# Kernel optimization log

Measured on AMD Instinct MI355X. Metric: run time of the kernel, lower is better.

The kernel has to match this reference:

```python
import jax, jax.numpy as jnp
import numpy as np
from jax import lax

D_MODEL = 768
BATCH = 16
SEQ = 2048
N_BLOCKS = D_MODEL // 3
LN_EPS = 1e-5


def setup_inputs() -> dict:
    key = jax.random.key(0)
    ks = jax.random.split(key, 4)
    scale = 1.0 / np.sqrt(D_MODEL)
    x = jax.random.normal(ks[0], (BATCH, SEQ, D_MODEL), dtype=jnp.float32)
    W_biv = jax.random.normal(ks[1], (D_MODEL, D_MODEL), dtype=jnp.float32) * scale
    b_biv = jnp.zeros((D_MODEL,), dtype=jnp.float32)
    W_decay = jax.random.normal(ks[2], (1, D_MODEL), dtype=jnp.float32) * scale
    b_decay = jnp.full((1,), 1.4, dtype=jnp.float32)  # nn.init.constant_(decay_proj.bias, 1.4)
    W_in = jax.random.normal(ks[3], (D_MODEL, D_MODEL), dtype=jnp.float32) * scale
    b_in = jnp.zeros((D_MODEL,), dtype=jnp.float32)
    ln_gamma = jnp.ones((D_MODEL,), dtype=jnp.float32)
    ln_beta = jnp.zeros((D_MODEL,), dtype=jnp.float32)
    return {"x": x, "W_biv": W_biv, "b_biv": b_biv, "W_decay": W_decay,
            "b_decay": b_decay, "W_in": W_in, "b_in": b_in,
            "ln_gamma": ln_gamma, "ln_beta": ln_beta}


def _quat_rotate_blocks(h_blocks, biv):
    """h_blocks, biv: (batch, n_blocks, 3) -> rotated (batch, n_blocks, 3)."""
    norm_b = jnp.maximum(jnp.linalg.norm(biv, axis=-1, keepdims=True), 1e-8)
    half = norm_b * 0.5
    w = jnp.cos(half)[..., 0]
    s = (jnp.sin(half) / norm_b)[..., 0]
    # note the original maps bivector components in reversed order
    qx = s * biv[..., 2]
    qy = -s * biv[..., 1]
    qz = s * biv[..., 0]
    vx, vy, vz = h_blocks[..., 0], h_blocks[..., 1], h_blocks[..., 2]
    tx = 2.0 * (qy * vz - qz * vy)
    ty = 2.0 * (qz * vx - qx * vz)
    tz = 2.0 * (qx * vy - qy * vx)
    rx = vx + w * tx + (qy * tz - qz * ty)
    ry = vy + w * ty + (qz * tx - qx * tz)
    rz = vz + w * tz + (qx * ty - qy * tx)
    return jnp.stack([rx, ry, rz], axis=-1)


def reference(x, W_biv, b_biv, W_decay, b_decay, W_in, b_in, ln_gamma, ln_beta):
    B, S, D = x.shape
    nb = D // 3
    # precompute all per-timestep projections as big GEMMs
    biv = (jnp.einsum('bsd,ed->bse', x, W_biv) + b_biv).reshape(B, S, nb, 3)
    decay = jax.nn.sigmoid(jnp.einsum('bsd,ed->bse', x, W_decay) + b_decay)  # (B,S,1)
    inj = jnp.einsum('bsd,ed->bse', x, W_in) + b_in  # (B,S,D)

    def step(h, t):
        biv_t, decay_t, inj_t = t
        rot = _quat_rotate_blocks(h.reshape(B, nb, 3), biv_t).reshape(B, D)
        h_next = decay_t * rot + inj_t
        return h_next, h_next

    xs = (jnp.moveaxis(biv, 1, 0), jnp.moveaxis(decay, 1, 0), jnp.moveaxis(inj, 1, 0))
    h0 = jnp.zeros((B, D), dtype=x.dtype)
    _, out = lax.scan(step, h0, xs)  # (S,B,D)
    out = jnp.moveaxis(out, 0, 1)  # (B,S,D)

    mean = jnp.mean(out, axis=-1, keepdims=True)
    var = jnp.mean(jnp.square(out - mean), axis=-1, keepdims=True)
    normed = (out - mean) * lax.rsqrt(var + LN_EPS) * ln_gamma + ln_beta
    return normed + x
```

## Files before the change

### kernel.cpp

```cpp
#include <hip/hip_runtime.h>
#include <stdint.h>

#define D_MODEL 768
#define BATCH   16
#define SEQ     2048
#define M_ROWS  (BATCH * SEQ)
#define LN_EPS  1e-5f

#define CHUNKS  64
#define CLEN    (SEQ / CHUNKS)
#define PFB     8

typedef __attribute__((ext_vector_type(4))) float        f32x4;
typedef __attribute__((ext_vector_type(8))) __bf16       bf16x8;
typedef __attribute__((ext_vector_type(2))) unsigned int u32x2;

__device__ __forceinline__ unsigned short f2bf(float f) {
    union { float f; uint32_t u; } v; v.f = f;
    uint32_t u = v.u;
    uint32_t r = (u + 0x7FFFu + ((u >> 16) & 1u)) >> 16;
    return (unsigned short)r;
}
__device__ __forceinline__ float bf2f(unsigned short u) {
    union { uint32_t u; float f; } v; v.u = (uint32_t)u << 16; return v.f;
}
__device__ __forceinline__ float bfx(u32x2 v, int k) {
    unsigned int w = (k & 2) ? v[1] : v[0];
    return bf2f((unsigned short)(w >> ((k & 1) * 16)));
}

__device__ __forceinline__ void gload_lds16(const void* g, void* l) {
    __builtin_amdgcn_global_load_lds(
        (const __attribute__((address_space(1))) unsigned int*)g,
        (__attribute__((address_space(3))) unsigned int*)l,
        16, 0, 0);
}

__global__ __launch_bounds__(256) void k_conv_decay(
    const float* __restrict__ x, const float* __restrict__ Wd,
    const float* __restrict__ bd, unsigned short* __restrict__ xb,
    float* __restrict__ decay)
{
    int row = blockIdx.x;
    int i   = threadIdx.x;
    const float* xr = x + (size_t)row * D_MODEL;
    float v0 = xr[i], v1 = xr[i + 256], v2 = xr[i + 512];
    unsigned short* xbr = xb + (size_t)row * D_MODEL;
    xbr[i] = f2bf(v0); xbr[i + 256] = f2bf(v1); xbr[i + 512] = f2bf(v2);

    float part = v0 * Wd[i] + v1 * Wd[i + 256] + v2 * Wd[i + 512];
    #pragma unroll
    for (int off = 32; off; off >>= 1) part += __shfl_down(part, off);
    __shared__ float wsum[4];
    int wid = i >> 6, lane = i & 63;
    if (lane == 0) wsum[wid] = part;
    __syncthreads();
    if (i == 0) {
        float s = wsum[0] + wsum[1] + wsum[2] + wsum[3] + bd[0];
        decay[row] = 1.f / (1.f + __expf(-s));
    }
}

__global__ __launch_bounds__(256) void k_conv_w(
    const float* __restrict__ Wb, const float* __restrict__ Wi,
    unsigned short* __restrict__ Wdst)
{
    const int NW = D_MODEL * D_MODEL;
    int g = blockIdx.x * 256 + threadIdx.x;
    int base = g * 4;
    unsigned short* dst = Wdst + base;
    const float* src;
    if (base < NW) { src = Wb + base; }
    else           { src = Wi + (base - NW); }
    float4 v = *(const float4*)src;
    ushort4 o;
    o.x = f2bf(v.x); o.y = f2bf(v.y); o.z = f2bf(v.z); o.w = f2bf(v.w);
    *(ushort4*)dst = o;
}

#define GBM 256
#define GBN 256
#define GNBX 6
#define GNBY 128

__global__ __launch_bounds__(512, 2) void k_gemm_fused(
    const unsigned short* __restrict__ A,
    const unsigned short* __restrict__ Bw,
    const float* __restrict__ bias_biv, const float* __restrict__ bias_in,
    u32x2* __restrict__ bivq, u32x2* __restrict__ injq)
{
    extern __shared__ unsigned short LDSBUF[];
    unsigned short* LA = LDSBUF;
    unsigned short* LB = LDSBUF + 32768;

    int id  = blockIdx.x;
    int swz = (id & 7) * 96 + (id >> 3);
    int bxc = swz % GNBX, byr = swz / GNBX;
    int m0 = byr * GBM, n0 = bxc * GBN;

    int tid  = threadIdx.x;
    int wid  = tid >> 6, lane = tid & 63;
    int wm = wid >> 2, wn = wid & 3;
    int rl = lane & 15, kq = lane >> 4;
    int sl = kq ^ ((rl >> 1) & 3);
    int aoff = (wm * 128 + rl) * 32 + sl * 8;
    int boff = (wn * 64  + rl) * 32 + sl * 8;

    f32x4 acc[8][4] = {};
    bf16x8 bfv[4];

    #define STAGE_UNIT(DBUF, KT, H, RH) do {                                     \
        int idx = (RH) * 512 + tid;                                              \
        int row = idx >> 2;                                                      \
        int ss  = ((idx & 3) ^ ((idx >> 3) & 3)) * 8;      \
        gload_lds16(A  + (size_t)(m0 + row) * D_MODEL + (KT) * 64 + (H) * 32 + ss, \
                    LA + (DBUF) * 16384 + (H) * 8192 + idx * 8);                 \
        gload_lds16(Bw + (size_t)(n0 + row) * D_MODEL + (KT) * 64 + (H) * 32 + ss, \
                    LB + (DBUF) * 16384 + (H) * 8192 + idx * 8);                 \
    } while (0)

    #define SUBPHASE(D, H, MH, DOSTAGE, SKT, SH, SRH, WAITSTR) do {              \
        const unsigned short* pa = LA + (D) * 16384 + (H) * 8192 + aoff + (MH) * 2048; \
        const unsigned short* pb = LB + (D) * 16384 + (H) * 8192 + boff;         \
        bf16x8 af[4];                                                            \
        _Pragma("unroll")                                                        \
        for (int i = 0; i < 4; ++i) af[i] = *(const bf16x8*)(pa + i * 512);      \
        if ((MH) == 0) {                                                         \
            _Pragma("unroll")                                                    \
            for (int j = 0; j < 4; ++j) bfv[j] = *(const bf16x8*)(pb + j * 512); \
        }                                                                        \
        if (DOSTAGE) STAGE_UNIT((D) ^ 1, SKT, SH, SRH);                          \
        asm volatile(WAITSTR ::: "memory");                                      \
        asm volatile("s_barrier" ::: "memory");                                  \
        asm volatile("s_waitcnt lgkmcnt(0)" ::: "memory");                       \
        __builtin_amdgcn_sched_barrier(0);                                       \
        __builtin_amdgcn_s_setprio(1);                                           \
        _Pragma("unroll")                                                        \
        for (int i = 0; i < 4; ++i)                                              \
            _Pragma("unroll")                                                    \
            for (int j = 0; j < 4; ++j)                                          \
                acc[(MH) * 4 + i][j] = __builtin_amdgcn_mfma_f32_16x16x32_bf16(  \
                    af[i], bfv[j], acc[(MH) * 4 + i][j], 0, 0, 0);               \
        __builtin_amdgcn_s_setprio(0);                                           \
        asm volatile("s_barrier" ::: "memory");                                  \
    } while (0)

    STAGE_UNIT(0, 0, 0, 0);
    STAGE_UNIT(0, 0, 0, 1);
    STAGE_UNIT(0, 0, 1, 0);
    STAGE_UNIT(0, 0, 1, 1);
    asm volatile("s_waitcnt vmcnt(4)" ::: "memory");
    asm volatile("s_barrier" ::: "memory");

    for (int kt = 0; kt < 10; ++kt) {
        int D = kt & 1;
        SUBPHASE(D, 0, 0, true, kt + 1, 0, 0, "");
        SUBPHASE(D, 0, 1, true, kt + 1, 0, 1, "s_waitcnt vmcnt(4)");
        SUBPHASE(D, 1, 0, true, kt + 1, 1, 0, "");
        SUBPHASE(D, 1, 1, true, kt + 1, 1, 1, "s_waitcnt vmcnt(4)");
    }
    SUBPHASE(0, 0, 0, true, 11, 0, 0, "");
    SUBPHASE(0, 0, 1, true, 11, 0, 1, "s_waitcnt vmcnt(4)");
    SUBPHASE(0, 1, 0, true, 11, 1, 0, "");
    SUBPHASE(0, 1, 1, true, 11, 1, 1, "s_waitcnt vmcnt(4)");
    SUBPHASE(1, 0, 0, false, 0, 0, 0, "");
    SUBPHASE(1, 0, 1, false, 0, 0, 0, "s_waitcnt vmcnt(0)");
    SUBPHASE(1, 1, 0, false, 0, 0, 0, "");
    SUBPHASE(1, 1, 1, false, 0, 0, 0, "");

    #undef SUBPHASE
    #undef STAGE_UNIT

    u32x2* Cq; const float* bias; int nloc;
    if (n0 < D_MODEL) { Cq = bivq; bias = bias_biv; nloc = n0; }
    else              { Cq = injq; bias = bias_in;  nloc = n0 - D_MODEL; }
    int cl = lane & 15;
    int qbase = (m0 >> 2) + wm * 32 + (lane >> 4);
    #pragma unroll
    for (int j = 0; j < 4; ++j) {
        int col = nloc + wn * 64 + j * 16 + cl;
        float bs = bias[col];
        #pragma unroll
        for (int i = 0; i < 8; ++i) {
            f32x4 a = acc[i][j];
            unsigned int lo = (unsigned int)f2bf(a[0] + bs) | ((unsigned int)f2bf(a[1] + bs) << 16);
            unsigned int hi = (unsigned int)f2bf(a[2] + bs) | ((unsigned int)f2bf(a[3] + bs) << 16);
            u32x2 pk = {lo, hi};
            Cq[(size_t)(qbase + i * 4) * D_MODEL + col] = pk;
        }
    }
}

#define QSTEP_CORE(BX,BY,BZ, IX,IY,IZ, DD)                              \
    {   float n2   = (BX)*(BX) + (BY)*(BY) + (BZ)*(BZ);                 \
        float nrm  = fmaxf(__builtin_sqrtf(n2), 1e-8f);                 \
        float half = 0.5f * nrm;                                        \
        float w = __cosf(half);                                         \
        float s = __sinf(half) / nrm;                                   \
        float qx = s * (BZ), qy = -s * (BY), qz = s * (BX);             \
        float tx = 2.f * (qy * hz - qz * hy);                           \
        float ty = 2.f * (qz * hx - qx * hz);                           \
        float tz = 2.f * (qx * hy - qy * hx);                           \
        float rx = hx + w * tx + (qy * tz - qz * ty);                   \
        float ry = hy + w * ty + (qz * tx - qx * tz);                   \
        float rz = hz + w * tz + (qx * ty - qy * tx);                   \
        hx = fmaf((DD), rx, (IX));                                      \
        hy = fmaf((DD), ry, (IY));                                      \
        hz = fmaf((DD), rz, (IZ));                                      \
        float nQw = w * Qw - qx * Qx - qy * Qy - qz * Qz;               \
        float nQx = w * Qx + Qw * qx + (qy * Qz - qz * Qy);             \
        float nQy = w * Qy + Qw * qy + (qz * Qx - qx * Qz);             \
        float nQz = w * Qz + Qw * qz + (qx * Qy - qy * Qx);             \
        Qw = nQw; Qx = nQx; Qy = nQy; Qz = nQz;                         \
        S *= (DD);                                                      \
    }

#define QSTEP_H(BX,BY,BZ, IX,IY,IZ, DD)                                 \
    {   float n2   = (BX)*(BX) + (BY)*(BY) + (BZ)*(BZ);                 \
        float nrm  = fmaxf(__builtin_sqrtf(n2), 1e-8f);                 \
        float half = 0.5f * nrm;                                        \
        float w = __cosf(half);                                         \
        float s = __sinf(half) / nrm;                                   \
        float qx = s * (BZ), qy = -s * (BY), qz = s * (BX);             \
        float tx = 2.f * (qy * hz - qz * hy);                           \
        float ty = 2.f * (qz * hx - qx * hz);                           \
        float tz = 2.f * (qx * hy - qy * hx);                           \
        float rx = hx + w * tx + (qy * tz - qz * ty);                   \
        float ry = hy + w * ty + (qz * tx - qx * tz);                   \
        float rz = hz + w * tz + (qx * ty - qy * tx);                   \
        hx = fmaf((DD), rx, (IX));                                      \
        hy = fmaf((DD), ry, (IY));                                      \
        hz = fmaf((DD), rz, (IZ));                                      \
    }

__global__ __launch_bounds__(256) void k_scan_p1(
    const u32x2* __restrict__ bivq, const u32x2* __restrict__ injq,
    const float* __restrict__ decay,
    float* __restrict__ ops)
{
    int j = threadIdx.x;
    int c = blockIdx.x & (CHUNKS - 1);
    int b = blockIdx.x >> 6;
    size_t qrow = ((size_t)b * SEQ + (size_t)c * CLEN) >> 2;
    const u32x2* bv = bivq + qrow * D_MODEL + 3 * j;
    const u32x2* ij = injq + qrow * D_MODEL + 3 * j;
    const float* dk = decay + (size_t)b * SEQ + c * CLEN;

    u32x2 Ab0, Ab1, Ab2, Ai0, Ai1, Ai2; f32x4 Ad;
    u32x2 Bb0, Bb1, Bb2, Bi0, Bi1, Bi2; f32x4 Bd;

    #define LOADQ1(P, q)                                                  \
        P##b0 = bv[(size_t)(q) * D_MODEL + 0];                            \
        P##b1 = bv[(size_t)(q) * D_MODEL + 1];                            \
        P##b2 = bv[(size_t)(q) * D_MODEL + 2];                            \
        P##i0 = ij[(size_t)(q) * D_MODEL + 0];                            \
        P##i1 = ij[(size_t)(q) * D_MODEL + 1];                            \
        P##i2 = ij[(size_t)(q) * D_MODEL + 2];                            \
        P##d  = *(const f32x4*)(dk + (q) * 4);

    #define PROC41(P)                                                     \
        _Pragma("unroll")                                                 \
        for (int k = 0; k < 4; ++k) {                                     \
            float bx = bfx(P##b0, k), by = bfx(P##b1, k), bz = bfx(P##b2, k); \
            float ix = bfx(P##i0, k), iy = bfx(P##i1, k), iz = bfx(P##i2, k); \
            float d = P##d[k];                                            \
            QSTEP_CORE(bx, by, bz, ix, iy, iz, d)                         \
        }

    float hx = 0.f, hy = 0.f, hz = 0.f;
    float Qw = 1.f, Qx = 0.f, Qy = 0.f, Qz = 0.f, S = 1.f;

    LOADQ1(A, 0)
    LOADQ1(B, 1)
    #pragma unroll
    for (int q0 = 0; q0 < CLEN / 4; q0 += 2) {
        PROC41(A)
        if (q0 + 2 < CLEN / 4) { LOADQ1(A, q0 + 2) }
        PROC41(B)
        if (q0 + 3 < CLEN / 4) { LOADQ1(B, q0 + 3) }
    }
    #undef LOADQ1
    #undef PROC41

    float* op = ops + ((size_t)(b * CHUNKS + c) * 256 + j) * 8;
    f32x4 o0 = {Qw, Qx, Qy, Qz};
    f32x4 o1 = {S, hx, hy, hz};
    *(f32x4*)op = o0;
    *(f32x4*)(op + 4) = o1;
}

__global__ __launch_bounds__(64) void k_scan_p2(
    const float* __restrict__ ops, unsigned short* __restrict__ hsb)
{
    int gid = blockIdx.x * 64 + threadIdx.x;
    int j = gid & 255, b = gid >> 8;

    float q0[PFB], q1[PFB], q2[PFB], q3[PFB], sc[PFB], o0[PFB], o1[PFB], o2[PFB];
    #pragma unroll
    for (int p = 0; p < PFB; ++p) {
        const float* op = ops + ((size_t)(b * CHUNKS + p) * 256 + j) * 8;
        f32x4 a = *(const f32x4*)op, bb = *(const f32x4*)(op + 4);
        q0[p] = a[0]; q1[p] = a[1]; q2[p] = a[2]; q3[p] = a[3];
        sc[p] = bb[0]; o0[p] = bb[1]; o1[p] = bb[2]; o2[p] = bb[3];
    }
    float hx = 0.f, hy = 0.f, hz = 0.f;
    for (int c0 = 0; c0 < CHUNKS; c0 += PFB) {
        #pragma unroll
        for (int p = 0; p < PFB; ++p) {
            int c = c0 + p;
            unsigned short* h = hsb + ((size_t)(b * CHUNKS + c) * 256 + j) * 3;
            h[0] = f2bf(hx); h[1] = f2bf(hy); h[2] = f2bf(hz);
            float w = q0[p], qx = q1[p], qy = q2[p], qz = q3[p];
            float s = sc[p], bx = o0[p], by = o1[p], bz = o2[p];
            int cn = c + PFB;
            if (cn < CHUNKS) {
                const float* op = ops + ((size_t)(b * CHUNKS + cn) * 256 + j) * 8;
                f32x4 a = *(const f32x4*)op, bb = *(const f32x4*)(op + 4);
                q0[p] = a[0]; q1[p] = a[1]; q2[p] = a[2]; q3[p] = a[3];
                sc[p] = bb[0]; o0[p] = bb[1]; o1[p] = bb[2]; o2[p] = bb[3];
            }
            float tx = 2.f * (qy * hz - qz * hy);
            float ty = 2.f * (qz * hx - qx * hz);
            float tz = 2.f * (qx * hy - qy * hx);
            float rx = hx + w * tx + (qy * tz - qz * ty);
            float ry = hy + w * ty + (qz * tx - qx * tz);
            float rz = hz + w * tz + (qx * ty - qy * tx);
            hx = fmaf(s, rx, bx);
            hy = fmaf(s, ry, by);
            hz = fmaf(s, rz, bz);
        }
    }
}

__global__ __launch_bounds__(256) void k_scan_p3(
    const u32x2* __restrict__ bivq, const u32x2* __restrict__ injq,
    const float* __restrict__ decay, const unsigned short* __restrict__ hsb,
    const unsigned short* __restrict__ xb, const float* __restrict__ gamma,
    const float* __restrict__ beta, float* __restrict__ out)
{
    int blk = blockIdx.x;
    int c = blk & (CHUNKS - 1);
    int b = blk >> 6;
    int j = threadIdx.x;
    size_t row0 = (size_t)b * SEQ + (size_t)c * CLEN;
    size_t qrow = row0 >> 2;
    const u32x2* bv = bivq + qrow * D_MODEL + 3 * j;
    const u32x2* ij = injq + qrow * D_MODEL + 3 * j;
    const float* dk = decay + row0;
    const unsigned short* h0p = hsb + ((size_t)(b * CHUNKS + c) * 256 + j) * 3;
    float hx = bf2f(h0p[0]), hy = bf2f(h0p[1]), hz = bf2f(h0p[2]);

    __shared__ uint32_t       hxyS[CLEN * 256];
    __shared__ unsigned short hzS [CLEN * 256];

    u32x2 Ab0, Ab1, Ab2, Ai0, Ai1, Ai2; f32x4 Ad;
    u32x2 Bb0, Bb1, Bb2, Bi0, Bi1, Bi2; f32x4 Bd;

    #define LOADQH(P, q)                                                  \
        P##b0 = bv[(size_t)(q) * D_MODEL + 0];                            \
        P##b1 = bv[(size_t)(q) * D_MODEL + 1];                            \
        P##b2 = bv[(size_t)(q) * D_MODEL + 2];                            \
        P##i0 = ij[(size_t)(q) * D_MODEL + 0];                            \
        P##i1 = ij[(size_t)(q) * D_MODEL + 1];                            \
        P##i2 = ij[(size_t)(q) * D_MODEL + 2];                            \
        P##d  = *(const f32x4*)(dk + (q) * 4);

    #define PROC4H(P, QBASE)                                              \
        _Pragma("unroll")                                                 \
        for (int k = 0; k < 4; ++k) {                                     \
            float bx = bfx(P##b0, k), by = bfx(P##b1, k), bz = bfx(P##b2, k); \
            float ix = bfx(P##i0, k), iy = bfx(P##i1, k), iz = bfx(P##i2, k); \
            float d = P##d[k];                                            \
            QSTEP_H(bx, by, bz, ix, iy, iz, d)                            \
            int tt = (QBASE) * 4 + k;                                     \
            hxyS[tt * 256 + j] = (uint32_t)f2bf(hx) | ((uint32_t)f2bf(hy) << 16); \
            hzS [tt * 256 + j] = f2bf(hz);                                \
        }

    LOADQH(A, 0)
    LOADQH(B, 1)
    #pragma unroll
    for (int q0 = 0; q0 < CLEN / 4; q0 += 2) {
        PROC4H(A, q0)
        if (q0 + 2 < CLEN / 4) { LOADQH(A, q0 + 2) }
        PROC4H(B, q0 + 1)
        if (q0 + 3 < CLEN / 4) { LOADQH(B, q0 + 3) }
    }
    #undef LOADQH
    #undef PROC4H

    __syncthreads();

    int wid = j >> 6, lane = j & 63;
    const float4* g4 = (const float4*)(gamma + lane * 12);
    const float4* e4 = (const float4*)(beta  + lane * 12);
    float4 G0 = g4[0], G1 = g4[1], G2 = g4[2];
    float4 E0 = e4[0], E1 = e4[1], E2 = e4[2];
    const unsigned short* xbase = xb  + row0 * D_MODEL;
    float*                obase = out + row0 * D_MODEL;

    for (int r = wid; r < CLEN; r += 4) {
        uint4   hv = *(const uint4*)  &hxyS[r * 256 + 4 * lane];
        ushort4 zv = *(const ushort4*)&hzS [r * 256 + 4 * lane];
        float h[12];
        h[0]  = bf2f((unsigned short)(hv.x & 0xFFFF)); h[1]  = bf2f((unsigned short)(hv.x >> 16)); h[2]  = bf2f(zv.x);
        h[3]  = bf2f((unsigned short)(hv.y & 0xFFFF)); h[4]  = bf2f((unsigned short)(hv.y >> 16)); h[5]  = bf2f(zv.y);
        h[6]  = bf2f((unsigned short)(hv.z & 0xFFFF)); h[7]  = bf2f((unsigned short)(hv.z >> 16)); h[8]  = bf2f(zv.z);
        h[9]  = bf2f((unsigned short)(hv.w & 0xFFFF)); h[10] = bf2f((unsigned short)(hv.w >> 16)); h[11] = bf2f(zv.w);
        float sp = 0.f, qp = 0.f;
        #pragma unroll
        for (int k = 0; k < 12; ++k) { sp += h[k]; qp += h[k] * h[k]; }
        #pragma unroll
        for (int off = 1; off < 64; off <<= 1) {
            sp += __shfl_xor(sp, off);
            qp += __shfl_xor(qp, off);
        }
        float mean = sp * (1.f / 768.f);
        float var  = qp * (1.f / 768.f) - mean * mean;
        float rstd = rsqrtf(var + LN_EPS);

        const unsigned short* xr2 = xbase + (size_t)r * D_MODEL + lane * 12;
        float*                or2 = obase + (size_t)r * D_MODEL + lane * 12;
        ushort4 Xa = *(const ushort4*)(xr2 + 0);
        ushort4 Xb = *(const ushort4*)(xr2 + 4);
        ushort4 Xc = *(const ushort4*)(xr2 + 8);
        float4 O0, O1, O2;
        O0.x = (h[0]  - mean) * rstd * G0.x + E0.x + bf2f(Xa.x);
        O0.y = (h[1]  - mean) * rstd * G0.y + E0.y + bf2f(Xa.y);
        O0.z = (h[2]  - mean) * rstd * G0.z + E0.z + bf2f(Xa.z);
        O0.w = (h[3]  - mean) * rstd * G0.w + E0.w + bf2f(Xa.w);
        O1.x = (h[4]  - mean) * rstd * G1.x + E1.x + bf2f(Xb.x);
        O1.y = (h[5]  - mean) * rstd * G1.y + E1.y + bf2f(Xb.y);
        O1.z = (h[6]  - mean) * rstd * G1.z + E1.z + bf2f(Xb.z);
        O1.w = (h[7]  - mean) * rstd * G1.w + E1.w + bf2f(Xb.w);
        O2.x = (h[8]  - mean) * rstd * G2.x + E2.x + bf2f(Xc.x);
        O2.y = (h[9]  - mean) * rstd * G2.y + E2.y + bf2f(Xc.y);
        O2.z = (h[10] - mean) * rstd * G2.z + E2.z + bf2f(Xc.z);
        O2.w = (h[11] - mean) * rstd * G2.w + E2.w + bf2f(Xc.w);
        *(float4*)(or2 + 0) = O0;
        *(float4*)(or2 + 4) = O1;
        *(float4*)(or2 + 8) = O2;
    }
}

extern "C" void kernel_launch(void* const* d_in, const int* in_sizes, int n_in,
                              void* d_out, int out_size, void* d_ws, size_t ws_size,
                              hipStream_t stream) {
    const float* x     = (const float*)d_in[0];
    const float* W_biv = (const float*)d_in[1];
    const float* b_biv = (const float*)d_in[2];
    const float* W_dec = (const float*)d_in[3];
    const float* b_dec = (const float*)d_in[4];
    const float* W_in  = (const float*)d_in[5];
    const float* b_in  = (const float*)d_in[6];
    const float* gamma = (const float*)d_in[7];
    const float* beta  = (const float*)d_in[8];
    float* out = (float*)d_out;

    char* ws = (char*)d_ws;
    unsigned short* xb    = (unsigned short*)(ws);
    unsigned short* Wcat  = (unsigned short*)(ws + 50331648);
    float*          decay = (float*)         (ws + 52690944);
    u32x2*          bivq  = (u32x2*)         (ws + 52822016);
    u32x2*          injq  = (u32x2*)         (ws + 103153664);
    float*          ops   = (float*)d_out;
    unsigned short* hsb   = (unsigned short*)(ws + 50331648);

    (void)in_sizes; (void)n_in; (void)out_size; (void)ws_size;

    hipFuncSetAttribute((const void*)k_gemm_fused,
                        hipFuncAttributeMaxDynamicSharedMemorySize, 131072);

    k_conv_decay<<<M_ROWS, 256, 0, stream>>>(x, W_dec, b_dec, xb, decay);
    k_conv_w    <<<1152,   256, 0, stream>>>(W_biv, W_in, Wcat);
    k_gemm_fused<<<GNBX * GNBY, 512, 131072, stream>>>(xb, Wcat, b_biv, b_in, bivq, injq);
    k_scan_p1   <<<1024, 256, 0, stream>>>(bivq, injq, decay, ops);
    k_scan_p2   <<<64,   64,  0, stream>>>(ops, hsb);
    k_scan_p3   <<<1024, 256, 0, stream>>>(bivq, injq, decay, hsb, xb, gamma, beta, out);
}
```

Before: 210.7 us.

## Shrink GEMM tile to 128x128 with triple-buffered 32-wide K pipeline

Restructures the fused bf16 GEMM from 256x256 tiles with 512 threads and double-buffered 64-wide K steps to 128x128 tiles with 256 threads, static LDS and a three-stage ring buffer of 32-wide K slices. The goal is higher occupancy (three blocks per CU) and a deeper prefetch distance to hide global-load latency, plus more blocks for better load balance across CUs. The cost is lower arithmetic intensity per tile, so more global and LDS traffic per FLOP, and more barriers per unit of work.

Result: slower. 219.3 us (+4.1%).

```diff
diff --git a/kernel.cpp b/kernel.cpp
--- a/kernel.cpp
+++ b/kernel.cpp
@@ -78,58 +78,56 @@
     *(ushort4*)dst = o;
 }
 
-#define GBM 256
-#define GBN 256
-#define GNBX 6
-#define GNBY 128
-
-__global__ __launch_bounds__(512, 2) void k_gemm_fused(
+#define G3NBX 12
+#define G3NBY 256
+#define NKT   24
+
+__global__ __launch_bounds__(256, 3) void k_gemm_fused(
     const unsigned short* __restrict__ A,
     const unsigned short* __restrict__ Bw,
     const float* __restrict__ bias_biv, const float* __restrict__ bias_in,
     u32x2* __restrict__ bivq, u32x2* __restrict__ injq)
 {
-    extern __shared__ unsigned short LDSBUF[];
-    unsigned short* LA = LDSBUF;
-    unsigned short* LB = LDSBUF + 32768;
+    __shared__ unsigned short LA[3 * 128 * 32];
+    __shared__ unsigned short LB[3 * 128 * 32];
 
     int id  = blockIdx.x;
-    int swz = (id & 7) * 96 + (id >> 3);
-    int bxc = swz % GNBX, byr = swz / GNBX;
-    int m0 = byr * GBM, n0 = bxc * GBN;
+    int swz = (id & 7) * 384 + (id >> 3);
+    int bxc = swz % G3NBX, byr = swz / G3NBX;
+    int m0 = byr * 128, n0 = bxc * 128;
 
     int tid  = threadIdx.x;
     int wid  = tid >> 6, lane = tid & 63;
-    int wm = wid >> 2, wn = wid & 3;
+    int wm = wid >> 1, wn = wid & 1;
     int rl = lane & 15, kq = lane >> 4;
     int sl = kq ^ ((rl >> 1) & 3);
-    int aoff = (wm * 128 + rl) * 32 + sl * 8;
-    int boff = (wn * 64  + rl) * 32 + sl * 8;
-
-    f32x4 acc[8][4] = {};
-    bf16x8 bfv[4];
-
-    #define STAGE_UNIT(DBUF, KT, H, RH) do {                                     \
-        int idx = (RH) * 512 + tid;                                              \
-        int row = idx >> 2;                                                      \
-        int ss  = ((idx & 3) ^ ((idx >> 3) & 3)) * 8;      \
-        gload_lds16(A  + (size_t)(m0 + row) * D_MODEL + (KT) * 64 + (H) * 32 + ss, \
-                    LA + (DBUF) * 16384 + (H) * 8192 + idx * 8);                 \
-        gload_lds16(Bw + (size_t)(n0 + row) * D_MODEL + (KT) * 64 + (H) * 32 + ss, \
-                    LB + (DBUF) * 16384 + (H) * 8192 + idx * 8);                 \
+    int aoff = (wm * 64 + rl) * 32 + sl * 8;
+    int boff = (wn * 64 + rl) * 32 + sl * 8;
+
+    f32x4 acc[4][4] = {};
+
+    #define STAGE_T(BUF, KT) do {                                                \
+        _Pragma("unroll")                                                        \
+        for (int p = 0; p < 2; ++p) {                                            \
+            int idx = p * 256 + tid;                                             \
+            int row = idx >> 2;                                                  \
+            int ss  = ((idx & 3) ^ ((idx >> 3) & 3)) * 8;  \
+            gload_lds16(A  + (size_t)(m0 + row) * D_MODEL + (KT) * 32 + ss,      \
+                        LA + (BUF) * 4096 + idx * 8);                            \
+            gload_lds16(Bw + (size_t)(n0 + row) * D_MODEL + (KT) * 32 + ss,      \
+                        LB + (BUF) * 4096 + idx * 8);                            \
+        }                                                                        \
     } while (0)
 
-    #define SUBPHASE(D, H, MH, DOSTAGE, SKT, SH, SRH, WAITSTR) do {              \
-        const unsigned short* pa = LA + (D) * 16384 + (H) * 8192 + aoff + (MH) * 2048; \
-        const unsigned short* pb = LB + (D) * 16384 + (H) * 8192 + boff;         \
-        bf16x8 af[4];                                                            \
+    #define PHASE3(KT, DOSTAGE, WAITSTR) do {                                    \
+        const unsigned short* pa = LA + ((KT) % 3) * 4096 + aoff;                \
+        const unsigned short* pb = LB + ((KT) % 3) * 4096 + boff;                \
+        bf16x8 af[4], bfv[4];                                                    \
         _Pragma("unroll")                                                        \
-        for (int i = 0; i < 4; ++i) af[i] = *(const bf16x8*)(pa + i * 512);      \
-        if ((MH) == 0) {                                                         \
-            _Pragma("unroll")                                                    \
-            for (int j = 0; j < 4; ++j) bfv[j] = *(const bf16x8*)(pb + j * 512); \
-        }                                                                        \
-        if (DOSTAGE) STAGE_UNIT((D) ^ 1, SKT, SH, SRH);                          \
+        for (int i = 0; i < 4; ++i) af[i]  = *(const bf16x8*)(pa + i * 512);     \
+        _Pragma("unroll")                                                        \
+        for (int j = 0; j < 4; ++j) bfv[j] = *(const bf16x8*)(pb + j * 512);     \
+        if (DOSTAGE) STAGE_T(((KT) + 2) % 3, (KT) + 2);                          \
         asm volatile(WAITSTR ::: "memory");                                      \
         asm volatile("s_barrier" ::: "memory");                                  \
         asm volatile("s_waitcnt lgkmcnt(0)" ::: "memory");                       \
@@ -139,49 +137,37 @@
         for (int i = 0; i < 4; ++i)                                              \
             _Pragma("unroll")                                                    \
             for (int j = 0; j < 4; ++j)                                          \
-                acc[(MH) * 4 + i][j] = __builtin_amdgcn_mfma_f32_16x16x32_bf16(  \
-                    af[i], bfv[j], acc[(MH) * 4 + i][j], 0, 0, 0);               \
+                acc[i][j] = __builtin_amdgcn_mfma_f32_16x16x32_bf16(             \
+                    af[i], bfv[j], acc[i][j], 0, 0, 0);                          \
         __builtin_amdgcn_s_setprio(0);                                           \
         asm volatile("s_barrier" ::: "memory");                                  \
     } while (0)
 
-    STAGE_UNIT(0, 0, 0, 0);
-    STAGE_UNIT(0, 0, 0, 1);
-    STAGE_UNIT(0, 0, 1, 0);
-    STAGE_UNIT(0, 0, 1, 1);
+    STAGE_T(0, 0);
+    STAGE_T(1, 1);
     asm volatile("s_waitcnt vmcnt(4)" ::: "memory");
     asm volatile("s_barrier" ::: "memory");
 
-    for (int kt = 0; kt < 10; ++kt) {
-        int D = kt & 1;
-        SUBPHASE(D, 0, 0, true, kt + 1, 0, 0, "");
-        SUBPHASE(D, 0, 1, true, kt + 1, 0, 1, "s_waitcnt vmcnt(4)");
-        SUBPHASE(D, 1, 0, true, kt + 1, 1, 0, "");
-        SUBPHASE(D, 1, 1, true, kt + 1, 1, 1, "s_waitcnt vmcnt(4)");
-    }
-    SUBPHASE(0, 0, 0, true, 11, 0, 0, "");
-    SUBPHASE(0, 0, 1, true, 11, 0, 1, "s_waitcnt vmcnt(4)");
-    SUBPHASE(0, 1, 0, true, 11, 1, 0, "");
-    SUBPHASE(0, 1, 1, true, 11, 1, 1, "s_waitcnt vmcnt(4)");
-    SUBPHASE(1, 0, 0, false, 0, 0, 0, "");
-    SUBPHASE(1, 0, 1, false, 0, 0, 0, "s_waitcnt vmcnt(0)");
-    SUBPHASE(1, 1, 0, false, 0, 0, 0, "");
-    SUBPHASE(1, 1, 1, false, 0, 0, 0, "");
-
-    #undef SUBPHASE
-    #undef STAGE_UNIT
+    #pragma unroll
+    for (int kt = 0; kt < NKT - 2; ++kt)
+        PHASE3(kt, true, "s_waitcnt vmcnt(4)");
+    PHASE3(NKT - 2, false, "s_waitcnt vmcnt(0)");
+    PHASE3(NKT - 1, false, "");
+
+    #undef PHASE3
+    #undef STAGE_T
 
     u32x2* Cq; const float* bias; int nloc;
     if (n0 < D_MODEL) { Cq = bivq; bias = bias_biv; nloc = n0; }
     else              { Cq = injq; bias = bias_in;  nloc = n0 - D_MODEL; }
     int cl = lane & 15;
-    int qbase = (m0 >> 2) + wm * 32 + (lane >> 4);
+    int qbase = (m0 >> 2) + wm * 16 + kq;
     #pragma unroll
     for (int j = 0; j < 4; ++j) {
         int col = nloc + wn * 64 + j * 16 + cl;
         float bs = bias[col];
         #pragma unroll
-        for (int i = 0; i < 8; ++i) {
+        for (int i = 0; i < 4; ++i) {
             f32x4 a = acc[i][j];
             unsigned int lo = (unsigned int)f2bf(a[0] + bs) | ((unsigned int)f2bf(a[1] + bs) << 16);
             unsigned int hi = (unsigned int)f2bf(a[2] + bs) | ((unsigned int)f2bf(a[3] + bs) << 16);
@@ -468,12 +454,9 @@
 
     (void)in_sizes; (void)n_in; (void)out_size; (void)ws_size;
 
-    hipFuncSetAttribute((const void*)k_gemm_fused,
-                        hipFuncAttributeMaxDynamicSharedMemorySize, 131072);
-
     k_conv_decay<<<M_ROWS, 256, 0, stream>>>(x, W_dec, b_dec, xb, decay);
     k_conv_w    <<<1152,   256, 0, stream>>>(W_biv, W_in, Wcat);
-    k_gemm_fused<<<GNBX * GNBY, 512, 131072, stream>>>(xb, Wcat, b_biv, b_in, bivq, injq);
+    k_gemm_fused<<<G3NBX * G3NBY, 256, 0, stream>>>(xb, Wcat, b_biv, b_in, bivq, injq);
     k_scan_p1   <<<1024, 256, 0, stream>>>(bivq, injq, decay, ops);
     k_scan_p2   <<<64,   64,  0, stream>>>(ops, hsb);
     k_scan_p3   <<<1024, 256, 0, stream>>>(bivq, injq, decay, hsb, xb, gamma, beta, out);
```
